# Kernel optimization log

Hardware: AMD Instinct MI355X
Metric: run time of the kernel (lower is better)

Reference implementation:

```python
import jax, jax.numpy as jnp
import numpy as np

B, S, D = 2, 2048, 512
E, K = 8, 2
H = 4 * D  # expert_dim
EPS = 1e-10


def setup_inputs() -> dict:
    key = jax.random.key(0)
    ks = jax.random.split(key, 5)
    scale = 1.0 / np.sqrt(D)
    return {
        "x": jax.random.normal(ks[0], (B, S, D), dtype=jnp.float32),
        "w_router": jax.random.normal(ks[1], (D, E), dtype=jnp.float32) * scale,
        "w_gate": jax.random.normal(ks[2], (D, E * H), dtype=jnp.float32) * scale,
        "w_up": jax.random.normal(ks[3], (D, E * H), dtype=jnp.float32) * scale,
        "w_down": jax.random.normal(ks[4], (H, D), dtype=jnp.float32) * (1.0 / np.sqrt(H)),
    }


def reference(x, w_router, w_gate, w_up, w_down):
    b, s, d = x.shape
    n = b * s
    xf = x.reshape(n, d)

    # Router: softmax over experts, pick top-k, renormalize
    router_probs = jax.nn.softmax(xf @ w_router, axis=-1)          # [N, E]
    top_p, top_i = jax.lax.top_k(router_probs, K)                  # [N, K]
    top_p = top_p / (top_p.sum(axis=-1, keepdims=True) + EPS)

    # Dense all-expert gate/up projections (as in original module)
    gate = jax.nn.silu(xf @ w_gate).reshape(n, E, H)               # [N, E, H]
    up = (xf @ w_up).reshape(n, E, H)                              # [N, E, H]

    # Gather per-token top-k expert slices and combine
    sel_gate = jnp.take_along_axis(gate, top_i[:, :, None], axis=1)  # [N, K, H]
    sel_up = jnp.take_along_axis(up, top_i[:, :, None], axis=1)      # [N, K, H]
    combined = jnp.sum(top_p[:, :, None] * sel_gate * sel_up, axis=1)  # [N, H]

    out = (combined @ w_down).reshape(b, s, d)

    # Load-balancing aux loss
    expert_probs = router_probs.mean(axis=0)                       # [E]
    lb_loss = E * jnp.sum(expert_probs * jnp.log(expert_probs * E + EPS))
    return out, lb_loss
```

## Files before the change

kernel.cpp:

```cpp
#include <hip/hip_runtime.h>
#include <hip/hip_bf16.h>

#define N_TOK 4096
#define D_DIM 512
#define E_NUM 8
#define H_DIM 2048
#define RB_NUM 256
#define TP_NUM 8704

typedef __attribute__((ext_vector_type(8))) short short8;
typedef __attribute__((ext_vector_type(4))) float f32x4;

__device__ inline short f2bs(float f) {
  __hip_bfloat16 h = __float2bfloat16(f);
  return *reinterpret_cast<short*>(&h);
}

__device__ inline void llds16(const short* g, short* l) {
  __builtin_amdgcn_global_load_lds(
      (const __attribute__((address_space(1))) void*)g,
      (__attribute__((address_space(3))) void*)l, 16, 0, 0);
}

__global__ void __launch_bounds__(256) prep_router_kernel(
    const float* __restrict__ wg, const float* __restrict__ wu,
    const float* __restrict__ wd, const float* __restrict__ x,
    const float* __restrict__ wr, short* __restrict__ wgb,
    short* __restrict__ wub, short* __restrict__ wdb, short* __restrict__ xb,
    int* __restrict__ cnt_blk, int* __restrict__ tok_bkt,
    float* __restrict__ p_bkt, float* __restrict__ psum_blk) {
  int u = blockIdx.x;
  int tid = threadIdx.x;

  if (u >= RB_NUM) {
    __shared__ float tbuf[64][33];
    int v = u - RB_NUM;
    const float* in;
    short* op;
    int R, C, c0, r0;
    if (v < 8192) {
      in = (v < 4096) ? wg : wu;
      op = (v < 4096) ? wgb : wub;
      int w = v & 4095;
      R = D_DIM; C = E_NUM * H_DIM;
      c0 = (w & 511) * 32; r0 = (w >> 9) * 64;
    } else {
      in = wd; op = wdb;
      int w = v - 8192;
      R = H_DIM; C = D_DIM;
      c0 = (w & 15) * 32; r0 = (w >> 4) * 64;
    }
    int cx = tid & 7, ry = tid >> 3;
#pragma unroll
    for (int p = 0; p < 2; ++p) {
      int row = ry + 32 * p;
      float4 vv = *(const float4*)&in[(size_t)(r0 + row) * C + c0 + cx * 4];
      tbuf[row][cx * 4 + 0] = vv.x;
      tbuf[row][cx * 4 + 1] = vv.y;
      tbuf[row][cx * 4 + 2] = vv.z;
      tbuf[row][cx * 4 + 3] = vv.w;
    }
    __syncthreads();
    int tx = tid & 31, ty = tid >> 5;
#pragma unroll
    for (int i = 0; i < 4; ++i) {
      int cl = ty + 8 * i;
      unsigned lo = (unsigned short)f2bs(tbuf[2 * tx][cl]);
      unsigned hi = (unsigned short)f2bs(tbuf[2 * tx + 1][cl]);
      ((int*)op)[(((size_t)(c0 + cl) * R) + r0) / 2 + tx] = (int)(lo | (hi << 16));
    }
    return;
  }

  __shared__ float wr_t[E_NUM * D_DIM];
  __shared__ int h_cnt[E_NUM];
  __shared__ float psh[E_NUM];
  int rb = u;
  for (int i = tid; i < D_DIM * E_NUM; i += 256)
    wr_t[(i & 7) * D_DIM + (i >> 3)] = wr[i];
  if (tid < E_NUM) { h_cnt[tid] = 0; psh[tid] = 0.f; }
  __syncthreads();

  int r = tid >> 4, pp = tid & 15;
  int t = rb * 16 + r;
  const float* xr0 = x + (size_t)t * D_DIM;
  short* xw0 = xb + (size_t)t * D_DIM;
  float acc[8] = {0, 0, 0, 0, 0, 0, 0, 0};
#pragma unroll
  for (int j = 0; j < 8; ++j) {
    int d = j * 64 + pp * 4;
    float4 xv = *(const float4*)(xr0 + d);
    short4 o;
    o.x = f2bs(xv.x); o.y = f2bs(xv.y); o.z = f2bs(xv.z); o.w = f2bs(xv.w);
    *(short4*)(xw0 + d) = o;
#pragma unroll
    for (int e = 0; e < 8; ++e) {
      float4 w = *(const float4*)&wr_t[e * D_DIM + d];
      acc[e] += xv.x * w.x + xv.y * w.y + xv.z * w.z + xv.w * w.w;
    }
  }
#pragma unroll
  for (int e = 0; e < 8; ++e) {
    acc[e] += __shfl_xor(acc[e], 1);
    acc[e] += __shfl_xor(acc[e], 2);
    acc[e] += __shfl_xor(acc[e], 4);
    acc[e] += __shfl_xor(acc[e], 8);
  }

  if (pp == 0) {
    float m = acc[0];
#pragma unroll
    for (int e = 1; e < 8; ++e) m = fmaxf(m, acc[e]);
    float p[8], s = 0.f;
#pragma unroll
    for (int e = 0; e < 8; ++e) { p[e] = expf(acc[e] - m); s += p[e]; }
    float inv = 1.f / s;
#pragma unroll
    for (int e = 0; e < 8; ++e) {
      p[e] *= inv;
      atomicAdd(&psh[e], p[e]);
    }
    int i0 = 0;
#pragma unroll
    for (int e = 1; e < 8; ++e) if (p[e] > p[i0]) i0 = e;
    int i1 = (i0 == 0) ? 1 : 0;
#pragma unroll
    for (int e = 0; e < 8; ++e) if (e != i0 && p[e] > p[i1]) i1 = e;
    float ps = p[i0] + p[i1] + 1e-10f;
    float q0 = p[i0] / ps, q1 = p[i1] / ps;
    int l0 = atomicAdd(&h_cnt[i0], 1);
    int l1 = atomicAdd(&h_cnt[i1], 1);
    tok_bkt[i0 * (RB_NUM * 16) + rb * 16 + l0] = t * 2 + 0;
    p_bkt[i0 * (RB_NUM * 16) + rb * 16 + l0] = q0;
    tok_bkt[i1 * (RB_NUM * 16) + rb * 16 + l1] = t * 2 + 1;
    p_bkt[i1 * (RB_NUM * 16) + rb * 16 + l1] = q1;
  }
  __syncthreads();
  if (tid < E_NUM) {
    cnt_blk[rb * 8 + tid] = h_cnt[tid];
    psum_blk[rb * 8 + tid] = psh[tid];
  }
}

__global__ void __launch_bounds__(256) route_pack_kernel(
    const int* __restrict__ cnt_blk, const int* __restrict__ tok_bkt,
    const float* __restrict__ p_bkt, int* __restrict__ dense_tok,
    float* __restrict__ dense_p, int* __restrict__ n_tot) {
  int e = blockIdx.x >> 4;
  int chunk = blockIdx.x & 15;
  int tid = threadIdx.x, lane = tid & 63, wid = tid >> 6;
  __shared__ int wsum[4];
  __shared__ int s_excl[16];
  __shared__ int s_cnt[16];
  int c = cnt_blk[tid * 8 + e];
  int inc = c;
#pragma unroll
  for (int ofs = 1; ofs < 64; ofs <<= 1) {
    int v = __shfl_up(inc, ofs);
    if (lane >= ofs) inc += v;
  }
  if (lane == 63) wsum[wid] = inc;
  __syncthreads();
  int pre = 0;
#pragma unroll
  for (int w = 0; w < 4; ++w) pre += (w < wid) ? wsum[w] : 0;
  int excl = inc + pre - c;
  if ((tid >> 4) == chunk) {
    s_excl[tid & 15] = excl;
    s_cnt[tid & 15] = c;
  }
  if (chunk == 0 && tid == 255) n_tot[e] = inc + pre;
  __syncthreads();
  int rbl = tid >> 4, i = tid & 15;
  int rb = chunk * 16 + rbl;
  if (i < s_cnt[rbl]) {
    int src = e * (RB_NUM * 16) + rb * 16 + i;
    int dst = e * N_TOK + s_excl[rbl] + i;
    dense_tok[dst] = tok_bkt[src];
    dense_p[dst] = p_bkt[src];
  }
}

__global__ void __launch_bounds__(256, 2) moe_gateup_kernel(
    const short* __restrict__ xb, const short* __restrict__ wg,
    const short* __restrict__ wu, const int* __restrict__ dense_tok,
    const float* __restrict__ dense_p, const int* __restrict__ n_tot,
    const float* __restrict__ psum_blk, short* __restrict__ act,
    float* __restrict__ out_loss) {
  int e = blockIdx.z;
  int tid = threadIdx.x;

  if (e == 8) {
    if (blockIdx.x || blockIdx.y) return;
    __shared__ float sums[8];
    if (tid < 8) sums[tid] = 0.f;
    __syncthreads();
#pragma unroll
    for (int ee = 0; ee < 8; ++ee)
      atomicAdd(&sums[ee], psum_blk[tid * 8 + ee]);
    __syncthreads();
    if (tid == 0) {
      float lb = 0.f;
#pragma unroll
      for (int ee = 0; ee < 8; ++ee) {
        float pe = sums[ee] / (float)N_TOK;
        lb += pe * logf(pe * 8.f + 1e-10f);
      }
      out_loss[0] = 8.f * lb;
    }
    return;
  }

  int n_e = n_tot[e];
  int rt = blockIdx.y;
  if (rt * 256 >= n_e) return;
  int h0 = blockIdx.x * 64;

  __shared__ __align__(16) short As[256 * 64];
  __shared__ __align__(16) short Bgs[64 * 64];
  __shared__ __align__(16) short Bus[64 * 64];
  __shared__ int s_row[256];
  __shared__ float s_pr[256];

  int lane = tid & 63, wid = tid >> 6;

  {
    int r = rt * 256 + tid;
    int srow = -1;
    float spr = 0.f;
    if (r < n_e) {
      srow = dense_tok[e * N_TOK + r];
      spr = dense_p[e * N_TOK + r];
    }
    s_row[tid] = srow;
    s_pr[tid] = spr;
  }
  __syncthreads();

  int cg = (lane & 7) ^ (lane >> 3);
  const short* baseA[8];
  const short* baseB[4];
#pragma unroll
  for (int jj = 0; jj < 8; ++jj) {
    int r = wid * 64 + jj * 8 + (lane >> 3);
    int row = s_row[r];
    int t = (row < 0) ? 0 : (row >> 1);
    baseA[jj] = xb + (size_t)t * D_DIM + cg * 8;
  }
  short* ldsB;
  {
    const short* wB = ((wid & 2) ? wu : wg) + (size_t)e * H_DIM * D_DIM;
    int rb = (wid & 1) * 32;
    ldsB = ((wid & 2) ? Bus : Bgs) + rb * 64;
#pragma unroll
    for (int jj = 0; jj < 4; ++jj) {
      int h = h0 + rb + jj * 8 + (lane >> 3);
      baseB[jj] = wB + (size_t)h * D_DIM + cg * 8;
    }
  }

  int ml = lane & 15, quad = lane >> 4;
  int m0w = wid * 64;
  f32x4 accG[4][4], accU[4][4];
#pragma unroll
  for (int mf = 0; mf < 4; ++mf)
#pragma unroll
    for (int nf = 0; nf < 4; ++nf) {
      accG[mf][nf] = (f32x4){0, 0, 0, 0};
      accU[mf][nf] = (f32x4){0, 0, 0, 0};
    }

  for (int kt = 0; kt < D_DIM / 64; ++kt) {
    int kb = kt * 64;
#pragma unroll
    for (int jj = 0; jj < 8; ++jj)
      llds16(baseA[jj] + kb, As + wid * 4096 + jj * 512);
#pragma unroll
    for (int jj = 0; jj < 4; ++jj)
      llds16(baseB[jj] + kb, ldsB + jj * 512);
    __syncthreads();
#pragma unroll
    for (int ks = 0; ks < 2; ++ks) {
      int cs = ((quad + ks * 4) ^ (ml & 7)) * 8;
      short8 a[4], bg[4], bu[4];
#pragma unroll
      for (int mf = 0; mf < 4; ++mf)
        a[mf] = *(const short8*)&As[(m0w + mf * 16 + ml) * 64 + cs];
#pragma unroll
      for (int nf = 0; nf < 4; ++nf) {
        bg[nf] = *(const short8*)&Bgs[(nf * 16 + ml) * 64 + cs];
        bu[nf] = *(const short8*)&Bus[(nf * 16 + ml) * 64 + cs];
      }
#pragma unroll
      for (int mf = 0; mf < 4; ++mf)
#pragma unroll
        for (int nf = 0; nf < 4; ++nf) {
          accG[mf][nf] = __builtin_amdgcn_mfma_f32_16x16x32_bf16(a[mf], bg[nf], accG[mf][nf], 0, 0, 0);
          accU[mf][nf] = __builtin_amdgcn_mfma_f32_16x16x32_bf16(a[mf], bu[nf], accU[mf][nf], 0, 0, 0);
        }
    }
    __syncthreads();
  }

#pragma unroll
  for (int mf = 0; mf < 4; ++mf)
#pragma unroll
    for (int r = 0; r < 4; ++r) {
      int rl = m0w + mf * 16 + quad * 4 + r;
      int arow = s_row[rl];
      if (arow >= 0) {
        float pr = s_pr[rl];
#pragma unroll
        for (int nf = 0; nf < 4; ++nf) {
          float g = accG[mf][nf][r], u = accU[mf][nf][r];
          float val = pr * (g / (1.f + __expf(-g))) * u;
          act[(size_t)arow * H_DIM + h0 + nf * 16 + ml] = f2bs(val);
        }
      }
    }
}

__global__ void __launch_bounds__(256, 3) down_kernel(
    const short* __restrict__ act, const short* __restrict__ wd,
    float* __restrict__ partial) {
  __shared__ __align__(16) short As0[128 * 64];
  __shared__ __align__(16) short As1[128 * 64];
  __shared__ __align__(16) short Bs[128 * 64];
  int d0 = blockIdx.x * 128;
  int t0 = blockIdx.y * 128;
  int ksb = blockIdx.z;
  int tid = threadIdx.x, lane = tid & 63, wid = tid >> 6;
  int cg = (lane & 7) ^ (lane >> 3);

  const short* baseA[4];
  const short* baseB[4];
#pragma unroll
  for (int jj = 0; jj < 4; ++jj) {
    int r = wid * 32 + jj * 8 + (lane >> 3);
    baseA[jj] = act + (size_t)(2 * (t0 + r)) * H_DIM + cg * 8;
    int d = d0 + wid * 32 + jj * 8 + (lane >> 3);
    baseB[jj] = wd + (size_t)d * H_DIM + cg * 8;
  }

  int ml = lane & 15, quad = lane >> 4;
  int m0w = (wid & 1) * 64, n0w = (wid >> 1) * 64;
  f32x4 acc[4][4];
#pragma unroll
  for (int mf = 0; mf < 4; ++mf)
#pragma unroll
    for (int nf = 0; nf < 4; ++nf) acc[mf][nf] = (f32x4){0, 0, 0, 0};

  for (int j = 0; j < 8; ++j) {
    int hb = (ksb * 8 + j) * 64;
#pragma unroll
    for (int jj = 0; jj < 4; ++jj) {
      llds16(baseA[jj] + hb, As0 + wid * 2048 + jj * 512);
      llds16(baseA[jj] + H_DIM + hb, As1 + wid * 2048 + jj * 512);
      llds16(baseB[jj] + hb, Bs + wid * 2048 + jj * 512);
    }
    __syncthreads();
#pragma unroll
    for (int s = 0; s < 2; ++s) {
      const short* Asl = s ? As1 : As0;
#pragma unroll
      for (int ks = 0; ks < 2; ++ks) {
        int cs = ((quad + ks * 4) ^ (ml & 7)) * 8;
        short8 a[4], b[4];
#pragma unroll
        for (int mf = 0; mf < 4; ++mf)
          a[mf] = *(const short8*)&Asl[(m0w + mf * 16 + ml) * 64 + cs];
#pragma unroll
        for (int nf = 0; nf < 4; ++nf)
          b[nf] = *(const short8*)&Bs[(n0w + nf * 16 + ml) * 64 + cs];
#pragma unroll
        for (int mf = 0; mf < 4; ++mf)
#pragma unroll
          for (int nf = 0; nf < 4; ++nf)
            acc[mf][nf] = __builtin_amdgcn_mfma_f32_16x16x32_bf16(a[mf], b[nf], acc[mf][nf], 0, 0, 0);
      }
    }
    __syncthreads();
  }

  float* pout = partial + (size_t)ksb * N_TOK * D_DIM;
#pragma unroll
  for (int mf = 0; mf < 4; ++mf)
#pragma unroll
    for (int r = 0; r < 4; ++r) {
      int t = t0 + m0w + mf * 16 + quad * 4 + r;
#pragma unroll
      for (int nf = 0; nf < 4; ++nf)
        pout[(size_t)t * D_DIM + d0 + n0w + nf * 16 + ml] = acc[mf][nf][r];
    }
}

__global__ void __launch_bounds__(256) reduce_kernel(
    const float* __restrict__ partial, float* __restrict__ out) {
  int i = blockIdx.x * 256 + threadIdx.x;
  const int Q = N_TOK * D_DIM / 4;
  const float4* p = (const float4*)partial;
  float4 a = p[i], b = p[i + Q], c = p[i + 2 * Q], d = p[i + 3 * Q];
  float4 r = {a.x + b.x + c.x + d.x, a.y + b.y + c.y + d.y,
              a.z + b.z + c.z + d.z, a.w + b.w + c.w + d.w};
  ((float4*)out)[i] = r;
}

extern "C" void kernel_launch(void* const* d_in, const int* in_sizes, int n_in,
                              void* d_out, int out_size, void* d_ws, size_t ws_size,
                              hipStream_t stream) {
  const float* x = (const float*)d_in[0];
  const float* wr = (const float*)d_in[1];
  const float* wg = (const float*)d_in[2];
  const float* wu = (const float*)d_in[3];
  const float* wd = (const float*)d_in[4];
  float* out = (float*)d_out;

  char* ws = (char*)d_ws;
  size_t off = 0;
  auto alloc = [&](size_t bytes) {
    char* p = ws + off;
    off += (bytes + 255) & ~(size_t)255;
    return p;
  };
  short* xb = (short*)alloc((size_t)N_TOK * D_DIM * 2);
  short* wgb = (short*)alloc((size_t)E_NUM * H_DIM * D_DIM * 2);
  short* wub = (short*)alloc((size_t)E_NUM * H_DIM * D_DIM * 2);
  short* wdb = (short*)alloc((size_t)D_DIM * H_DIM * 2);
  short* act = (short*)alloc((size_t)N_TOK * 2 * H_DIM * 2);
  float* partial = (float*)alloc((size_t)4 * N_TOK * D_DIM * 4);
  int* cnt_blk = (int*)alloc((size_t)RB_NUM * E_NUM * 4);
  int* tok_bkt = (int*)alloc((size_t)E_NUM * RB_NUM * 16 * 4);
  float* p_bkt = (float*)alloc((size_t)E_NUM * RB_NUM * 16 * 4);
  float* psum_blk = (float*)alloc((size_t)RB_NUM * E_NUM * 4);
  int* dense_tok = (int*)alloc((size_t)E_NUM * N_TOK * 4);
  float* dense_p = (float*)alloc((size_t)E_NUM * N_TOK * 4);
  int* n_tot = (int*)alloc((size_t)E_NUM * 4);

  prep_router_kernel<<<RB_NUM + TP_NUM, 256, 0, stream>>>(
      wg, wu, wd, x, wr, wgb, wub, wdb, xb, cnt_blk, tok_bkt, p_bkt, psum_blk);
  route_pack_kernel<<<E_NUM * 16, 256, 0, stream>>>(
      cnt_blk, tok_bkt, p_bkt, dense_tok, dense_p, n_tot);
  moe_gateup_kernel<<<dim3(H_DIM / 64, N_TOK / 256, E_NUM + 1), 256, 0, stream>>>(
      xb, wgb, wub, dense_tok, dense_p, n_tot, psum_blk, act,
      out + (size_t)N_TOK * D_DIM);
  down_kernel<<<dim3(D_DIM / 128, N_TOK / 128, 4), 256, 0, stream>>>(
      act, wdb, partial);
  reduce_kernel<<<N_TOK * D_DIM / 4 / 256, 256, 0, stream>>>(partial, out);
}
```

Before: 204.7 us.

## Retile down-projection to 64 tokens by 256 output columns per block

The down-projection block tile changes from 128x128 to 64 tokens by 256 output features. Each wave now owns 64 output columns and all 64 tokens, and it accumulates both top-k slots into the same accumulators. The intent is to change the balance of A versus weight loads and to remove the per-wave M split. The cost is double the B tile in LDS, and per-wave MFMA work per load changes.

```diff
diff --git a/kernel.cpp b/kernel.cpp
--- a/kernel.cpp
+++ b/kernel.cpp
@@ -323,27 +323,33 @@
 __global__ void __launch_bounds__(256, 3) down_kernel(
     const short* __restrict__ act, const short* __restrict__ wd,
     float* __restrict__ partial) {
-  __shared__ __align__(16) short As0[128 * 64];
-  __shared__ __align__(16) short As1[128 * 64];
-  __shared__ __align__(16) short Bs[128 * 64];
-  int d0 = blockIdx.x * 128;
-  int t0 = blockIdx.y * 128;
+  __shared__ __align__(16) short As0[64 * 64];
+  __shared__ __align__(16) short As1[64 * 64];
+  __shared__ __align__(16) short Bs[256 * 64];
+  int d0 = blockIdx.x * 256;
+  int t0 = blockIdx.y * 64;
   int ksb = blockIdx.z;
   int tid = threadIdx.x, lane = tid & 63, wid = tid >> 6;
   int cg = (lane & 7) ^ (lane >> 3);
 
   const short* baseA[4];
-  const short* baseB[4];
+  const short* baseB[8];
+  int slot = wid >> 1;
+  int arow0 = (wid & 1) * 32;
 #pragma unroll
   for (int jj = 0; jj < 4; ++jj) {
-    int r = wid * 32 + jj * 8 + (lane >> 3);
-    baseA[jj] = act + (size_t)(2 * (t0 + r)) * H_DIM + cg * 8;
-    int d = d0 + wid * 32 + jj * 8 + (lane >> 3);
+    int r = arow0 + jj * 8 + (lane >> 3);
+    baseA[jj] = act + (size_t)(2 * (t0 + r) + slot) * H_DIM + cg * 8;
+  }
+#pragma unroll
+  for (int jj = 0; jj < 8; ++jj) {
+    int d = d0 + wid * 64 + jj * 8 + (lane >> 3);
     baseB[jj] = wd + (size_t)d * H_DIM + cg * 8;
   }
+  short* ldsA = (slot ? As1 : As0) + arow0 * 64;
 
   int ml = lane & 15, quad = lane >> 4;
-  int m0w = (wid & 1) * 64, n0w = (wid >> 1) * 64;
+  int n0w = wid * 64;
   f32x4 acc[4][4];
 #pragma unroll
   for (int mf = 0; mf < 4; ++mf)
@@ -353,31 +359,31 @@
   for (int j = 0; j < 8; ++j) {
     int hb = (ksb * 8 + j) * 64;
 #pragma unroll
-    for (int jj = 0; jj < 4; ++jj) {
-      llds16(baseA[jj] + hb, As0 + wid * 2048 + jj * 512);
-      llds16(baseA[jj] + H_DIM + hb, As1 + wid * 2048 + jj * 512);
-      llds16(baseB[jj] + hb, Bs + wid * 2048 + jj * 512);
-    }
-    __syncthreads();
-#pragma unroll
-    for (int s = 0; s < 2; ++s) {
-      const short* Asl = s ? As1 : As0;
-#pragma unroll
-      for (int ks = 0; ks < 2; ++ks) {
-        int cs = ((quad + ks * 4) ^ (ml & 7)) * 8;
-        short8 a[4], b[4];
-#pragma unroll
-        for (int mf = 0; mf < 4; ++mf)
-          a[mf] = *(const short8*)&Asl[(m0w + mf * 16 + ml) * 64 + cs];
-#pragma unroll
-        for (int nf = 0; nf < 4; ++nf)
-          b[nf] = *(const short8*)&Bs[(n0w + nf * 16 + ml) * 64 + cs];
-#pragma unroll
-        for (int mf = 0; mf < 4; ++mf)
-#pragma unroll
-          for (int nf = 0; nf < 4; ++nf)
-            acc[mf][nf] = __builtin_amdgcn_mfma_f32_16x16x32_bf16(a[mf], b[nf], acc[mf][nf], 0, 0, 0);
+    for (int jj = 0; jj < 4; ++jj)
+      llds16(baseA[jj] + hb, ldsA + jj * 512);
+#pragma unroll
+    for (int jj = 0; jj < 8; ++jj)
+      llds16(baseB[jj] + hb, Bs + wid * 4096 + jj * 512);
+    __syncthreads();
+#pragma unroll
+    for (int ks = 0; ks < 2; ++ks) {
+      int cs = ((quad + ks * 4) ^ (ml & 7)) * 8;
+      short8 a0[4], a1[4], b[4];
+#pragma unroll
+      for (int mf = 0; mf < 4; ++mf) {
+        a0[mf] = *(const short8*)&As0[(mf * 16 + ml) * 64 + cs];
+        a1[mf] = *(const short8*)&As1[(mf * 16 + ml) * 64 + cs];
       }
+#pragma unroll
+      for (int nf = 0; nf < 4; ++nf)
+        b[nf] = *(const short8*)&Bs[(n0w + nf * 16 + ml) * 64 + cs];
+#pragma unroll
+      for (int mf = 0; mf < 4; ++mf)
+#pragma unroll
+        for (int nf = 0; nf < 4; ++nf) {
+          acc[mf][nf] = __builtin_amdgcn_mfma_f32_16x16x32_bf16(a0[mf], b[nf], acc[mf][nf], 0, 0, 0);
+          acc[mf][nf] = __builtin_amdgcn_mfma_f32_16x16x32_bf16(a1[mf], b[nf], acc[mf][nf], 0, 0, 0);
+        }
     }
     __syncthreads();
   }
@@ -387,7 +393,7 @@
   for (int mf = 0; mf < 4; ++mf)
 #pragma unroll
     for (int r = 0; r < 4; ++r) {
-      int t = t0 + m0w + mf * 16 + quad * 4 + r;
+      int t = t0 + mf * 16 + quad * 4 + r;
 #pragma unroll
       for (int nf = 0; nf < 4; ++nf)
         pout[(size_t)t * D_DIM + d0 + n0w + nf * 16 + ml] = acc[mf][nf][r];
@@ -443,7 +449,7 @@
   moe_gateup_kernel<<<dim3(H_DIM / 64, N_TOK / 256, E_NUM + 1), 256, 0, stream>>>(
       xb, wgb, wub, dense_tok, dense_p, n_tot, psum_blk, act,
       out + (size_t)N_TOK * D_DIM);
-  down_kernel<<<dim3(D_DIM / 128, N_TOK / 128, 4), 256, 0, stream>>>(
+  down_kernel<<<dim3(D_DIM / 256, N_TOK / 64, 4), 256, 0, stream>>>(
       act, wdb, partial);
   reduce_kernel<<<N_TOK * D_DIM / 4 / 256, 256, 0, stream>>>(partial, out);
 }
```

After: 202.0 us, median of 2. No clear change (-1.3%).
